# Performance work log

Measured on AMD Instinct MI355X. Metric: run time of the kernel, lower is better.

Reference implementation:

```python
import jax, jax.numpy as jnp
import numpy as np

B, N, F = 64, 512, 128

def setup_inputs() -> dict:
    key = jax.random.key(0)
    k1, k2 = jax.random.split(key)
    inp = jax.random.normal(k1, (B, N, F), dtype=jnp.float32)
    valid_mask = jnp.ones((B, N, N), dtype=jnp.float32)
    weight = 0.1 * jax.random.normal(k2, (N, N), dtype=jnp.float32)
    return {"input": inp, "valid_mask": valid_mask, "weight": weight}

def reference(input, valid_mask, weight):
    # softmax over last dim of weight, broadcast over batch
    adj = jax.nn.softmax(weight, axis=-1)[None, :, :] * valid_mask  # [B,N,N]
    n = weight.shape[0]
    adj = adj + jnp.eye(n, dtype=adj.dtype)[None, :, :]
    # symmetric degree normalization D^-1/2 A D^-1/2 (D diagonal of row sums).
    # Original builds dense D and does two matmuls; diagonal scaling is the
    # identical math expressed as row/col broadcast.
    row_sum = adj.sum(axis=2)  # [B,N]
    d = jnp.where(row_sum > 0, jax.lax.rsqrt(row_sum), 0.0)  # inf -> 0 handling
    adj_nor = d[:, :, None] * adj * d[:, None, :]  # [B,N,N]
    return jnp.matmul(adj_nor, input)  # [B,N,F]
```

## Files before the change

kernel.cpp:

```cpp
#include <hip/hip_runtime.h>
#include <math.h>

#define BB 64
#define NN 512
#define FF 128

typedef __bf16 bf16x8 __attribute__((ext_vector_type(8)));
typedef float floatx4 __attribute__((ext_vector_type(4)));

__device__ __forceinline__ unsigned int bf16u(float f) {
    unsigned int u = __builtin_bit_cast(unsigned int, f);
    unsigned int r = (u + 0x7FFFu + ((u >> 16) & 1u)) >> 16;
    return r & 0xFFFFu;
}

__global__ __launch_bounds__(256) void softmax_kernel(const float* __restrict__ w,
                                                      float* __restrict__ S) {
    const int row = blockIdx.x;
    const float* wr = w + (size_t)row * NN;
    float* sr = S + (size_t)row * NN;
    const int tid = threadIdx.x;
    const int wave = tid >> 6, lane = tid & 63;

    float v0 = wr[tid];
    float v1 = wr[tid + 256];

    float m = fmaxf(v0, v1);
    #pragma unroll
    for (int off = 32; off > 0; off >>= 1)
        m = fmaxf(m, __shfl_down(m, off, 64));
    __shared__ float red[8];
    if (lane == 0) red[wave] = m;
    __syncthreads();
    if (tid == 0) red[4] = fmaxf(fmaxf(red[0], red[1]), fmaxf(red[2], red[3]));
    __syncthreads();
    m = red[4];

    float e0 = expf(v0 - m);
    float e1 = expf(v1 - m);

    float s = e0 + e1;
    #pragma unroll
    for (int off = 32; off > 0; off >>= 1)
        s += __shfl_down(s, off, 64);
    __syncthreads();
    if (lane == 0) red[wave] = s;
    __syncthreads();
    if (tid == 0) red[5] = 1.0f / (red[0] + red[1] + red[2] + red[3]);
    __syncthreads();
    const float inv = red[5];

    sr[tid]       = e0 * inv;
    sr[tid + 256] = e1 * inv;
}

__global__ __launch_bounds__(256) void rowsum_kernel(const float* __restrict__ S,
                                                     const float* __restrict__ mask,
                                                     float* __restrict__ dvec) {
    const int gwave = (int)((blockIdx.x * 256u + threadIdx.x) >> 6);
    const int lane = threadIdx.x & 63;
    const int b = gwave >> 9;
    const int i = gwave & (NN - 1);

    const float4* mrow = (const float4*)(mask + ((size_t)b * NN + i) * NN);
    const float4* srow = (const float4*)(S + (size_t)i * NN);

    float sum = 0.f;
    #pragma unroll
    for (int k = 0; k < 2; k++) {
        int idx = lane + k * 64;
        float4 mv = mrow[idx];
        float4 sv = srow[idx];
        sum += mv.x * sv.x + mv.y * sv.y + mv.z * sv.z + mv.w * sv.w;
    }
    #pragma unroll
    for (int off = 32; off > 0; off >>= 1)
        sum += __shfl_down(sum, off, 64);
    if (lane == 0) {
        float rs = sum + 1.0f;
        dvec[gwave] = (rs > 0.f) ? (1.0f / sqrtf(rs)) : 0.f;
    }
}

#define TI 32
#define TK 64
#define ASTR 72

__global__ __launch_bounds__(256) void matmul_kernel(const float* __restrict__ S,
                                                     const float* __restrict__ mask,
                                                     const float* __restrict__ dvec,
                                                     const float* __restrict__ in,
                                                     float* __restrict__ out) {
    __shared__ unsigned short Alds[TI * ASTR];
    __shared__ unsigned short Xlds[FF * ASTR];

    const int b = blockIdx.y;
    const int i_base = blockIdx.x * TI;
    const int tid = threadIdx.x;
    const int w = tid >> 6;
    const int lane = tid & 63;
    const int quad = lane >> 4;
    const int l16 = lane & 15;
    const int iw = (w & 1) * 16;
    const int fw = (w >> 1) * 64;

    const float* dB = dvec + b * NN;

    floatx4 acc[4];
    #pragma unroll
    for (int nt = 0; nt < 4; nt++) acc[nt] = (floatx4){0.f, 0.f, 0.f, 0.f};

    const int a_il = tid >> 3;
    const int a_js = (tid & 7) * 8;
    const int x_jl = tid & 63;
    const int x_f0 = (tid >> 6) * 32;

    for (int j0 = 0; j0 < NN; j0 += TK) {
        __syncthreads();

        {
            const float4* mrow = (const float4*)(mask + ((size_t)b * NN + i_base + a_il) * NN + j0 + a_js);
            const float4* srow = (const float4*)(S + (size_t)(i_base + a_il) * NN + j0 + a_js);
            float4 m0 = mrow[0], m1 = mrow[1];
            float4 s0 = srow[0], s1 = srow[1];
            uint4 pk;
            pk.x = bf16u(m0.x * s0.x) | (bf16u(m0.y * s0.y) << 16);
            pk.y = bf16u(m0.z * s0.z) | (bf16u(m0.w * s0.w) << 16);
            pk.z = bf16u(m1.x * s1.x) | (bf16u(m1.y * s1.y) << 16);
            pk.w = bf16u(m1.z * s1.z) | (bf16u(m1.w * s1.w) << 16);
            *((uint4*)&Alds[a_il * ASTR + a_js]) = pk;
        }

        {
            float dj = dB[j0 + x_jl];
            const float4* xp = (const float4*)(in + ((size_t)b * NN + j0 + x_jl) * FF + x_f0);
            #pragma unroll
            for (int c = 0; c < 8; c++) {
                float4 xv = xp[c];
                int fb = x_f0 + 4 * c;
                Xlds[(fb + 0) * ASTR + x_jl] = (unsigned short)bf16u(xv.x * dj);
                Xlds[(fb + 1) * ASTR + x_jl] = (unsigned short)bf16u(xv.y * dj);
                Xlds[(fb + 2) * ASTR + x_jl] = (unsigned short)bf16u(xv.z * dj);
                Xlds[(fb + 3) * ASTR + x_jl] = (unsigned short)bf16u(xv.w * dj);
            }
        }

        __syncthreads();

        #pragma unroll
        for (int s = 0; s < 2; s++) {
            bf16x8 af = *(const bf16x8*)&Alds[(iw + l16) * ASTR + s * 32 + quad * 8];
            #pragma unroll
            for (int nt = 0; nt < 4; nt++) {
                bf16x8 bfr = *(const bf16x8*)&Xlds[(fw + nt * 16 + l16) * ASTR + s * 32 + quad * 8];
                acc[nt] = __builtin_amdgcn_mfma_f32_16x16x32_bf16(af, bfr, acc[nt], 0, 0, 0);
            }
        }
    }

    #pragma unroll
    for (int nt = 0; nt < 4; nt++) {
        int f = fw + nt * 16 + l16;
        #pragma unroll
        for (int r = 0; r < 4; r++) {
            int i = i_base + iw + quad * 4 + r;
            float di = dB[i];
            float x = in[((size_t)b * NN + i) * FF + f];
            out[((size_t)b * NN + i) * FF + f] = di * (acc[nt][r] + di * x);
        }
    }
}

extern "C" void kernel_launch(void* const* d_in, const int* in_sizes, int n_in,
                              void* d_out, int out_size, void* d_ws, size_t ws_size,
                              hipStream_t stream) {
    const float* inp  = (const float*)d_in[0];
    const float* mask = (const float*)d_in[1];
    const float* w    = (const float*)d_in[2];
    float* out = (float*)d_out;

    float* S    = (float*)d_ws;
    float* dvec = S + (size_t)NN * NN;

    softmax_kernel<<<NN, 256, 0, stream>>>(w, S);
    rowsum_kernel<<<(BB * NN) / 4, 256, 0, stream>>>(S, mask, dvec);
    dim3 g3(NN / TI, BB);
    matmul_kernel<<<g3, 256, 0, stream>>>(S, mask, dvec, inp, out);
}
```

Before: 151.5 us.

## Pre-transpose scaled input to bf16 and double-buffer adjacency tiles in matmul

Adds a kernel that scales the input by the degree vector, converts it to bf16 and writes it transposed to workspace once per batch. Before, every one of the 16 row-tile blocks per batch redid that conversion through LDS. The matmul now reads B fragments straight from global memory and double-buffers the A tile in LDS, with the next chunk's loads issued before the MFMAs to overlap them. The rowsum kernel is regrouped to 16 lanes per row. In exchange it adds a kernel launch, extra workspace traffic, and global fragment loads that may be less efficient than LDS.

```diff
diff --git a/kernel.cpp b/kernel.cpp
--- a/kernel.cpp
+++ b/kernel.cpp
@@ -57,42 +57,81 @@
 __global__ __launch_bounds__(256) void rowsum_kernel(const float* __restrict__ S,
                                                      const float* __restrict__ mask,
                                                      float* __restrict__ dvec) {
-    const int gwave = (int)((blockIdx.x * 256u + threadIdx.x) >> 6);
-    const int lane = threadIdx.x & 63;
-    const int b = gwave >> 9;
-    const int i = gwave & (NN - 1);
+    const int b = blockIdx.x >> 5;
+    const int g = blockIdx.x & 31;
+    const int r = threadIdx.x >> 4;
+    const int l = threadIdx.x & 15;
+    const int i = g * 16 + r;
 
     const float4* mrow = (const float4*)(mask + ((size_t)b * NN + i) * NN);
     const float4* srow = (const float4*)(S + (size_t)i * NN);
 
     float sum = 0.f;
     #pragma unroll
-    for (int k = 0; k < 2; k++) {
-        int idx = lane + k * 64;
-        float4 mv = mrow[idx];
-        float4 sv = srow[idx];
+    for (int k = 0; k < 8; ++k) {
+        float4 mv = mrow[l + 16 * k];
+        float4 sv = srow[l + 16 * k];
         sum += mv.x * sv.x + mv.y * sv.y + mv.z * sv.z + mv.w * sv.w;
     }
     #pragma unroll
-    for (int off = 32; off > 0; off >>= 1)
-        sum += __shfl_down(sum, off, 64);
-    if (lane == 0) {
+    for (int off = 8; off > 0; off >>= 1)
+        sum += __shfl_down(sum, off, 16);
+    if (l == 0) {
         float rs = sum + 1.0f;
-        dvec[gwave] = (rs > 0.f) ? (1.0f / sqrtf(rs)) : 0.f;
+        dvec[b * NN + i] = (rs > 0.f) ? (1.0f / sqrtf(rs)) : 0.f;
+    }
+}
+
+#define PADT 129
+__global__ __launch_bounds__(256) void xt_kernel(const float* __restrict__ in,
+                                                 const float* __restrict__ dvec,
+                                                 unsigned short* __restrict__ Xt) {
+    __shared__ unsigned short T[64 * PADT];
+    const int b = blockIdx.y;
+    const int j0 = blockIdx.x * 64;
+    const int tid = threadIdx.x;
+
+    const int fg = tid & 31;
+    const int jr = tid >> 5;
+    #pragma unroll
+    for (int p = 0; p < 8; ++p) {
+        int j = jr + 8 * p;
+        float dj = dvec[b * NN + j0 + j];
+        float4 xv = *(const float4*)(in + ((size_t)b * NN + j0 + j) * FF + 4 * fg);
+        T[j * PADT + 4 * fg + 0] = (unsigned short)bf16u(xv.x * dj);
+        T[j * PADT + 4 * fg + 1] = (unsigned short)bf16u(xv.y * dj);
+        T[j * PADT + 4 * fg + 2] = (unsigned short)bf16u(xv.z * dj);
+        T[j * PADT + 4 * fg + 3] = (unsigned short)bf16u(xv.w * dj);
+    }
+    __syncthreads();
+
+    const int c = tid & 7;
+    const int fr = tid >> 3;
+    #pragma unroll
+    for (int q = 0; q < 4; ++q) {
+        int f = fr + 32 * q;
+        unsigned int v01 = (unsigned int)T[(8 * c + 0) * PADT + f] |
+                           ((unsigned int)T[(8 * c + 1) * PADT + f] << 16);
+        unsigned int v23 = (unsigned int)T[(8 * c + 2) * PADT + f] |
+                           ((unsigned int)T[(8 * c + 3) * PADT + f] << 16);
+        unsigned int v45 = (unsigned int)T[(8 * c + 4) * PADT + f] |
+                           ((unsigned int)T[(8 * c + 5) * PADT + f] << 16);
+        unsigned int v67 = (unsigned int)T[(8 * c + 6) * PADT + f] |
+                           ((unsigned int)T[(8 * c + 7) * PADT + f] << 16);
+        uint4 pk = make_uint4(v01, v23, v45, v67);
+        *(uint4*)(Xt + ((size_t)b * FF + f) * NN + j0 + 8 * c) = pk;
     }
 }
 
 #define TI 32
-#define TK 64
 #define ASTR 72
-
 __global__ __launch_bounds__(256) void matmul_kernel(const float* __restrict__ S,
                                                      const float* __restrict__ mask,
                                                      const float* __restrict__ dvec,
+                                                     const unsigned short* __restrict__ Xt,
                                                      const float* __restrict__ in,
                                                      float* __restrict__ out) {
-    __shared__ unsigned short Alds[TI * ASTR];
-    __shared__ unsigned short Xlds[FF * ASTR];
+    __shared__ __align__(16) unsigned short Alds[2][TI * ASTR];
 
     const int b = blockIdx.y;
     const int i_base = blockIdx.x * TI;
@@ -105,6 +144,7 @@
     const int fw = (w >> 1) * 64;
 
     const float* dB = dvec + b * NN;
+    const unsigned short* XtB = Xt + (size_t)b * FF * NN;
 
     floatx4 acc[4];
     #pragma unroll
@@ -112,49 +152,58 @@
 
     const int a_il = tid >> 3;
     const int a_js = (tid & 7) * 8;
-    const int x_jl = tid & 63;
-    const int x_f0 = (tid >> 6) * 32;
-
-    for (int j0 = 0; j0 < NN; j0 += TK) {
+    const float* mbase = mask + ((size_t)b * NN + i_base + a_il) * NN + a_js;
+    const float* sbase = S + (size_t)(i_base + a_il) * NN + a_js;
+    unsigned short* awr = &Alds[0][0] + a_il * ASTR + a_js;
+
+    {
+        float4 m0 = *(const float4*)(mbase);
+        float4 m1 = *(const float4*)(mbase + 4);
+        float4 s0 = *(const float4*)(sbase);
+        float4 s1 = *(const float4*)(sbase + 4);
+        uint4 pk;
+        pk.x = bf16u(m0.x * s0.x) | (bf16u(m0.y * s0.y) << 16);
+        pk.y = bf16u(m0.z * s0.z) | (bf16u(m0.w * s0.w) << 16);
+        pk.z = bf16u(m1.x * s1.x) | (bf16u(m1.y * s1.y) << 16);
+        pk.w = bf16u(m1.z * s1.z) | (bf16u(m1.w * s1.w) << 16);
+        *(uint4*)awr = pk;
+    }
+
+    #pragma unroll
+    for (int c = 0; c < 8; ++c) {
+        const int p = c & 1;
+        float4 m0, m1, s0, s1;
+        if (c < 7) {
+            int jn = (c + 1) * 64;
+            m0 = *(const float4*)(mbase + jn);
+            m1 = *(const float4*)(mbase + jn + 4);
+            s0 = *(const float4*)(sbase + jn);
+            s1 = *(const float4*)(sbase + jn + 4);
+        }
         __syncthreads();
 
-        {
-            const float4* mrow = (const float4*)(mask + ((size_t)b * NN + i_base + a_il) * NN + j0 + a_js);
-            const float4* srow = (const float4*)(S + (size_t)(i_base + a_il) * NN + j0 + a_js);
-            float4 m0 = mrow[0], m1 = mrow[1];
-            float4 s0 = srow[0], s1 = srow[1];
+        const int j0 = c * 64;
+        bf16x8 bfr[2][4];
+        #pragma unroll
+        for (int s = 0; s < 2; ++s)
+            #pragma unroll
+            for (int nt = 0; nt < 4; ++nt)
+                bfr[s][nt] = *(const bf16x8*)&XtB[(size_t)(fw + nt * 16 + l16) * NN + j0 + s * 32 + quad * 8];
+        #pragma unroll
+        for (int s = 0; s < 2; ++s) {
+            bf16x8 af = *(const bf16x8*)&Alds[p][(iw + l16) * ASTR + s * 32 + quad * 8];
+            #pragma unroll
+            for (int nt = 0; nt < 4; ++nt)
+                acc[nt] = __builtin_amdgcn_mfma_f32_16x16x32_bf16(af, bfr[s][nt], acc[nt], 0, 0, 0);
+        }
+
+        if (c < 7) {
             uint4 pk;
             pk.x = bf16u(m0.x * s0.x) | (bf16u(m0.y * s0.y) << 16);
             pk.y = bf16u(m0.z * s0.z) | (bf16u(m0.w * s0.w) << 16);
             pk.z = bf16u(m1.x * s1.x) | (bf16u(m1.y * s1.y) << 16);
             pk.w = bf16u(m1.z * s1.z) | (bf16u(m1.w * s1.w) << 16);
-            *((uint4*)&Alds[a_il * ASTR + a_js]) = pk;
-        }
-
-        {
-            float dj = dB[j0 + x_jl];
-            const float4* xp = (const float4*)(in + ((size_t)b * NN + j0 + x_jl) * FF + x_f0);
-            #pragma unroll
-            for (int c = 0; c < 8; c++) {
-                float4 xv = xp[c];
-                int fb = x_f0 + 4 * c;
-                Xlds[(fb + 0) * ASTR + x_jl] = (unsigned short)bf16u(xv.x * dj);
-                Xlds[(fb + 1) * ASTR + x_jl] = (unsigned short)bf16u(xv.y * dj);
-                Xlds[(fb + 2) * ASTR + x_jl] = (unsigned short)bf16u(xv.z * dj);
-                Xlds[(fb + 3) * ASTR + x_jl] = (unsigned short)bf16u(xv.w * dj);
-            }
-        }
-
-        __syncthreads();
-
-        #pragma unroll
-        for (int s = 0; s < 2; s++) {
-            bf16x8 af = *(const bf16x8*)&Alds[(iw + l16) * ASTR + s * 32 + quad * 8];
-            #pragma unroll
-            for (int nt = 0; nt < 4; nt++) {
-                bf16x8 bfr = *(const bf16x8*)&Xlds[(fw + nt * 16 + l16) * ASTR + s * 32 + quad * 8];
-                acc[nt] = __builtin_amdgcn_mfma_f32_16x16x32_bf16(af, bfr, acc[nt], 0, 0, 0);
-            }
+            *(uint4*)(&Alds[p ^ 1][0] + a_il * ASTR + a_js) = pk;
         }
     }
 
@@ -179,11 +228,14 @@
     const float* w    = (const float*)d_in[2];
     float* out = (float*)d_out;
 
-    float* S    = (float*)d_ws;
+    unsigned short* Xt = (unsigned short*)d_ws;
+    float* S    = (float*)(Xt + (size_t)BB * FF * NN);
     float* dvec = S + (size_t)NN * NN;
 
     softmax_kernel<<<NN, 256, 0, stream>>>(w, S);
-    rowsum_kernel<<<(BB * NN) / 4, 256, 0, stream>>>(S, mask, dvec);
+    rowsum_kernel<<<BB * 32, 256, 0, stream>>>(S, mask, dvec);
+    dim3 gx(NN / 64, BB);
+    xt_kernel<<<gx, 256, 0, stream>>>(inp, dvec, Xt);
     dim3 g3(NN / TI, BB);
-    matmul_kernel<<<g3, 256, 0, stream>>>(S, mask, dvec, inp, out);
-}
+    matmul_kernel<<<g3, 256, 0, stream>>>(S, mask, dvec, Xt, inp, out);
+}
```

New measurement: 154.2 us. About the same (+1.8%).
